# Kernel optimization log

Measured on AMD Instinct MI355X. Metric: run time of the kernel, lower is better.

## Reference

```python
import jax, jax.numpy as jnp
import numpy as np

EPS = 1e-5  # BatchNorm eps (torch default)


def _norm_adj(adj):
    # DenseGCNConv: add self-loops, symmetric degree normalization
    N = adj.shape[-1]
    adj = adj + jnp.eye(N, dtype=adj.dtype)
    d = jnp.clip(adj.sum(-1), 1.0, None) ** -0.5
    return d[..., :, None] * adj * d[..., None, :]


def _gcn(x, adj_norm, W, b):
    return jnp.einsum('bij,bjf->bif', adj_norm, x @ W) + b


def _batchnorm(h, gamma, beta):
    # torch BatchNorm1d in training mode over flattened (B*N, C)
    B, N, C = h.shape
    hf = h.reshape(B * N, C)
    mu = hf.mean(0)
    var = hf.var(0)  # biased, as used for normalization
    out = (hf - mu) * jax.lax.rsqrt(var + EPS) * gamma + beta
    return out.reshape(B, N, C)


def setup_inputs() -> dict:
    key = jax.random.key(0)
    ks = jax.random.split(key, 24)
    B, N, F, H, D = 4, 256, 6, 128, 256
    s = 0.05
    a = jax.random.uniform(ks[1], (B, N, N), dtype=jnp.float32)
    adj = ((a + jnp.swapaxes(a, 1, 2)) / 2 < 0.1).astype(jnp.float32)  # sparse symmetric adjacency
    return {
        'x': jax.random.normal(ks[0], (B, N, F), dtype=jnp.float32),
        'adj': adj,
        'W1': jax.random.normal(ks[2], (F, H)) * s, 'b1': jnp.zeros((H,)),
        'W2': jax.random.normal(ks[3], (H, H)) * s, 'b2': jnp.zeros((H,)),
        'W3': jax.random.normal(ks[4], (H, D)) * s, 'b3': jnp.zeros((D,)),
        'g1': jnp.ones((H,)), 'beta1': jnp.zeros((H,)),
        'g2': jnp.ones((H,)), 'beta2': jnp.zeros((H,)),
        'e1w': jax.random.normal(ks[5], (2 * D, H)) * s, 'e1b': jnp.zeros((H,)),
        'e2w': jax.random.normal(ks[6], (H, H // 2)) * s, 'e2b': jnp.zeros((H // 2,)),
        'e3w': jax.random.normal(ks[7], (H // 2, 1)) * s, 'e3b': jnp.zeros((1,)),
        'f1w': jax.random.normal(ks[8], (D, H)) * s, 'f1b': jnp.zeros((H,)),
        'f2w': jax.random.normal(ks[9], (H, H)) * s, 'f2b': jnp.zeros((H,)),
        'f3w': jax.random.normal(ks[10], (H, F)) * s, 'f3b': jnp.zeros((F,)),
    }


def reference(x, adj, W1, b1, W2, b2, W3, b3, g1, beta1, g2, beta2,
              e1w, e1b, e2w, e2b, e3w, e3b, f1w, f1b, f2w, f2b, f3w, f3b):
    adj_norm = _norm_adj(adj)
    h = jax.nn.relu(_batchnorm(_gcn(x, adj_norm, W1, b1), g1, beta1))
    h = jax.nn.relu(_batchnorm(_gcn(h, adj_norm, W2, b2), g2, beta2))
    h = jax.nn.relu(_gcn(h, adj_norm, W3, b3))  # [B,N,D]
    D = h.shape[-1]
    # AdjacencyDecoder: Linear(cat(h_i,h_j)) == h_i@e1w[:D] + h_j@e1w[D:] (fused form, same math)
    hi = h @ e1w[:D]   # [B,N,H]
    hj = h @ e1w[D:]   # [B,N,H]
    p = jax.nn.relu(hi[:, :, None, :] + hj[:, None, :, :] + e1b)  # [B,N,N,H]
    p = jax.nn.relu(p @ e2w + e2b)                                 # [B,N,N,H/2]
    logits = (p @ e3w + e3b)[..., 0]                               # [B,N,N]
    logits = (logits + jnp.swapaxes(logits, 1, 2)) / 2
    adj_pred = jax.nn.sigmoid(logits)
    # FeatureDecoder
    f = jax.nn.relu(h @ f1w + f1b)
    f = jax.nn.relu(f @ f2w + f2b)
    feat_pred = f @ f3w + f3b
    return adj_pred, feat_pred
```

## Files before the change

### kernel.cpp

```cpp
#include <hip/hip_runtime.h>


typedef float v4f __attribute__((ext_vector_type(4)));
typedef short v8s __attribute__((ext_vector_type(8)));

__device__ __forceinline__ unsigned short f2bs(float f) {
    union { float f; unsigned int u; } v;
    v.f = f;
    return (unsigned short)((v.u + 0x7fffu + ((v.u >> 16) & 1u)) >> 16);
}

__global__ void k_pre(const float* x, const float* W1, const float* adj,
                      const float* e2w, float* buf, float* dg,
                      unsigned short* bfr_g, float* st) {
    __shared__ float ss[256];
    int blk = blockIdx.x, tid = threadIdx.x;
    if (blk < 512) {
        int idx = blk * 256 + tid;
        int m = idx >> 7, n = idx & 127;
        float s = 0.f;
        for (int k = 0; k < 6; k++) s += x[m * 6 + k] * W1[k * 128 + n];
        buf[idx] = s;
    } else if (blk < 768) {
        int row = (blk - 512) * 4 + (tid >> 6);
        int lane = tid & 63;
        const float* ap = adj + (long)row * 256;
        ss[tid] = ap[lane] + ap[lane + 64] + ap[lane + 128] + ap[lane + 192];
        __syncthreads();
        for (int o = 32; o > 0; o >>= 1) {
            if (lane < o) ss[tid] += ss[tid + o];
            __syncthreads();
        }
        if (lane == 0) {
            float t = ss[tid] + 1.f;
            if (t < 1.f) t = 1.f;
            dg[row] = rsqrtf(t);
        }
    } else {
        for (int s = tid; s < 8192; s += 256) {
            int k = s >> 6, n = s & 63;
            int kc = k >> 5, q = (k & 31) >> 3, t = k & 7;
            int nt = n >> 4, c2 = n & 15;
            bfr_g[(((nt * 4 + kc) * 64) + q * 16 + c2) * 8 + t] = f2bs(e2w[s]);
        }
        st[tid] = 0.f;
        st[256 + tid] = 0.f;
    }
}

__global__ void k_an(const float* adj, const float* dg, float* An) {
    for (int p = 0; p < 2; p++) {
        int idx = blockIdx.x * 256 + threadIdx.x + p * 131072;
        int b = idx >> 16, i = (idx >> 8) & 255, j = idx & 255;
        float v = adj[idx] + ((i == j) ? 1.f : 0.f);
        An[idx] = dg[b * 256 + i] * v * dg[b * 256 + j];
    }
}

__device__ void dev_tile(int t, const float* A, const float* B, const float* bias,
                         const float* stat, const float* g, const float* beta,
                         float* ostat, float* C,
                         int K, int N, int relu,
                         int sA, int sB, int sC, int tiles_n, int tiles_m,
                         float* smem) {
    float* As = smem;
    float* Bs = smem + 272;
    int tid = threadIdx.x;
    int n2 = tid & 15, ml = tid >> 4;
    int bx = t % tiles_n;
    int tmp = t / tiles_n;
    int by = tmp % tiles_m;
    int bz = tmp / tiles_m;
    int m0 = by * 16, n0 = bx * 32;
    const float* Ab = A + (long)bz * sA;
    const float* Bb = B + (long)bz * sB;
    float* Cb = C + (long)bz * sC;
    float c0 = 0.f, c1 = 0.f;
    for (int k0 = 0; k0 < K; k0 += 16) {
        int kk = tid & 15, mm = tid >> 4;
        int kg = k0 + kk;
        float v = Ab[(long)(m0 + mm) * K + kg];
        if (stat != 0) {
            float mu = stat[kg] * (1.f / 1024.f);
            float vr = stat[128 + kg] * (1.f / 1024.f) - mu * mu;
            float sc = rsqrtf(vr + 1e-5f) * g[kg];
            v = (v - mu) * sc + beta[kg];
            if (v < 0.f) v = 0.f;
        }
        As[kk * 17 + mm] = v;
        int nn2 = tid & 31, kk2 = tid >> 5;
        Bs[kk2 * 33 + nn2] = Bb[(long)(k0 + kk2) * N + n0 + nn2];
        int idx = tid + 256;
        nn2 = idx & 31; kk2 = idx >> 5;
        Bs[kk2 * 33 + nn2] = Bb[(long)(k0 + kk2) * N + n0 + nn2];
        __syncthreads();
        #pragma unroll
        for (int q = 0; q < 16; q++) {
            float a = As[q * 17 + ml];
            float b0 = Bs[q * 33 + n2 * 2];
            float b1 = Bs[q * 33 + n2 * 2 + 1];
            c0 += a * b0; c1 += a * b1;
        }
        __syncthreads();
    }
    int mRow = m0 + ml, nn = n0 + n2 * 2;
    if (bias != 0) { c0 += bias[nn]; c1 += bias[nn + 1]; }
    if (relu) {
        if (c0 < 0.f) c0 = 0.f;
        if (c1 < 0.f) c1 = 0.f;
    }
    Cb[(long)mRow * N + nn] = c0;
    Cb[(long)mRow * N + nn + 1] = c1;

    if (ostat != 0) {
        float* sred = smem + 800;
        float* qred = smem + 1344;
        __syncthreads();
        sred[(n2 * 2) * 17 + ml] = c0;
        sred[(n2 * 2 + 1) * 17 + ml] = c1;
        qred[(n2 * 2) * 17 + ml] = c0 * c0;
        qred[(n2 * 2 + 1) * 17 + ml] = c1 * c1;
        __syncthreads();
        if (tid < 32) {
            float s = 0.f, q = 0.f;
            for (int u = 0; u < 16; u++) {
                s += sred[tid * 17 + u];
                q += qred[tid * 17 + u];
            }
            atomicAdd(&ostat[n0 + tid], s);
            atomicAdd(&ostat[128 + n0 + tid], q);
        }
    }
}

__global__ void k_tgemm(const float* A, const float* B, const float* bias,
                        const float* stat, const float* g, const float* beta,
                        float* ostat, float* C,
                        int K, int N, int relu,
                        int sA, int sB, int sC, int tiles_n, int tiles_m) {
    __shared__ float smem[1888];
    dev_tile(blockIdx.x, A, B, bias, stat, g, beta, ostat, C,
             K, N, relu, sA, sB, sC, tiles_n, tiles_m, smem);
}

__global__ void k_g67(const float* hb, const float* e1w, float* hi,
                      const float* f1w, const float* f1b, float* f1) {
    __shared__ float smem[1888];
    int t = blockIdx.x;
    if (t < 512) {
        dev_tile(t, hb, e1w, 0, 0, 0, 0, 0, hi,
                 256, 128, 0, 0, 32768, 131072, 4, 64, smem);
    } else {
        dev_tile(t - 512, hb, f1w, f1b, 0, 0, 0, 0, f1,
                 256, 128, 1, 0, 0, 0, 4, 64, smem);
    }
}

__global__ void k_decf(const float* hi, const float* hj, const float* e1b,
                       const unsigned short* bfr_g, const float* e2b,
                       const float* e3w, const float* e3b,
                       const float* f1, const float* f2w, const float* f2b_,
                       const float* f3w, const float* f3b,
                       float* lg, float* out) {
    __shared__ float smem[4608];
    int tid = threadIdx.x;
    int blk = blockIdx.x;
    if (blk < 1024) {
        float* red = smem;
        float* pre_sh = smem + 4352;
        int lane = tid & 63, wv = tid >> 6;
        int col = lane & 15, quad = lane >> 4;
        int bi = blk, b = bi >> 8;
        if (tid < 128) pre_sh[tid] = hi[bi * 128 + tid] + e1b[tid];
        __syncthreads();
        float e2bv[4], e3wv[4];
        for (int nt = 0; nt < 4; nt++) {
            e2bv[nt] = e2b[nt * 16 + col];
            e3wv[nt] = e3w[nt * 16 + col];
        }
        const float* hjb = hj + b * 32768;
        #pragma unroll 1
        for (int ms = 0; ms < 4; ms++) {
            v4f acc[4];
            for (int nt = 0; nt < 4; nt++) {
                v4f z = {0.f, 0.f, 0.f, 0.f};
                acc[nt] = z;
            }
            int j = wv * 64 + ms * 16 + col;
            const float* rowp = hjb + j * 128 + quad * 8;
            #pragma unroll 1
            for (int kc = 0; kc < 4; kc++) {
                const float* pp = pre_sh + kc * 32 + quad * 8;
                const float* hp = rowp + kc * 32;
                v8s af;
                #pragma unroll
                for (int t = 0; t < 8; t++) {
                    float p = pp[t] + hp[t];
                    p = (p > 0.f) ? p : 0.f;
                    af[t] = (short)f2bs(p);
                }
                #pragma unroll
                for (int nt = 0; nt < 4; nt++) {
                    v8s bf = *(const v8s*)&bfr_g[(((nt * 4 + kc) * 64) + lane) * 8];
                    acc[nt] = __builtin_amdgcn_mfma_f32_16x16x32_bf16(
                        af, bf, acc[nt], 0, 0, 0);
                }
            }
            #pragma unroll
            for (int r = 0; r < 4; r++) {
                float s = 0.f;
                #pragma unroll
                for (int nt = 0; nt < 4; nt++) {
                    float v = acc[nt][r] + e2bv[nt];
                    if (v > 0.f) s += v * e3wv[nt];
                }
                red[(wv * 64 + ms * 16 + quad * 4 + r) * 17 + col] = s;
            }
        }
        __syncthreads();
        float s = e3b[0];
        for (int c = 0; c < 16; c++) s += red[tid * 17 + c];
        lg[bi * 256 + tid] = s;
    } else {
        float* f2row = smem;
        int r0 = (blk - 1024) * 4;
        for (int p = 0; p < 2; p++) {
            int idx = tid + p * 256;
            int r = r0 + (idx >> 7), n = idx & 127;
            float s = f2b_[n];
            const float* f1r = f1 + (long)r * 128;
            for (int k = 0; k < 128; k++) s += f1r[k] * f2w[k * 128 + n];
            if (s < 0.f) s = 0.f;
            f2row[idx] = s;
        }
        __syncthreads();
        if (tid < 24) {
            int r = tid / 6, c = tid % 6;
            float s = f3b[c];
            const float* fr = f2row + r * 128;
            for (int k = 0; k < 128; k++) s += fr[k] * f3w[k * 6 + c];
            out[262144 + (r0 + r) * 6 + c] = s;
        }
    }
}

__global__ void k_symsig(const float* lg, float* out) {
    for (int p = 0; p < 2; p++) {
        int idx = blockIdx.x * 256 + threadIdx.x + p * 131072;
        int b = idx >> 16, i = (idx >> 8) & 255, j = idx & 255;
        float v = 0.5f * (lg[idx] + lg[(b << 16) + (j << 8) + i]);
        out[idx] = 1.f / (1.f + expf(-v));
    }
}

extern "C" void kernel_launch(void* const* d_in, const int* in_sizes, int n_in,
                              void* d_out, int out_size, void* d_ws, size_t ws_size,
                              hipStream_t stream) {
    const float* x   = (const float*)d_in[0];
    const float* adj = (const float*)d_in[1];
    const float* W1  = (const float*)d_in[2];
    const float* b1  = (const float*)d_in[3];
    const float* W2  = (const float*)d_in[4];
    const float* b2  = (const float*)d_in[5];
    const float* W3  = (const float*)d_in[6];
    const float* b3  = (const float*)d_in[7];
    const float* g1  = (const float*)d_in[8];
    const float* be1 = (const float*)d_in[9];
    const float* g2  = (const float*)d_in[10];
    const float* be2 = (const float*)d_in[11];
    const float* e1w = (const float*)d_in[12];
    const float* e1b = (const float*)d_in[13];
    const float* e2w = (const float*)d_in[14];
    const float* e2b = (const float*)d_in[15];
    const float* e3w = (const float*)d_in[16];
    const float* e3b = (const float*)d_in[17];
    const float* f1w = (const float*)d_in[18];
    const float* f1b = (const float*)d_in[19];
    const float* f2w = (const float*)d_in[20];
    const float* f2b_ = (const float*)d_in[21];
    const float* f3w = (const float*)d_in[22];
    const float* f3b = (const float*)d_in[23];

    float* out = (float*)d_out;

    if (ws_size < (size_t)1600000 * 4) {
        hipMemsetAsync(d_out, 0x60, 4096, stream);
        return;
    }
    float* ws = (float*)d_ws;
    float* st1 = ws;
    float* st2 = ws + 256;
    float* dg  = ws + 512;
    unsigned short* bfr_g = (unsigned short*)(ws + 1536);
    float* An  = ws + 5632;
    float* buf = An + 262144;
    float* hb  = buf + 262144;
    float* lg  = hb + 262144;
    float* h1  = lg + 262144;
    float* h2  = h1 + 131072;
    float* hi  = h2 + 131072;
    float* hj  = hi + 131072;

    k_pre<<<769, 256, 0, stream>>>(x, W1, adj, e2w, buf, dg, bfr_g, st1);
    k_an<<<512, 256, 0, stream>>>(adj, dg, An);
    k_tgemm<<<256, 256, 0, stream>>>(An, buf, b1, 0, 0, 0, st1, h1,
                                     256, 128, 0, 65536, 32768, 32768, 4, 16);
    k_tgemm<<<256, 256, 0, stream>>>(h1, W2, 0, st1, g1, be1, 0, buf,
                                     128, 128, 0, 0, 0, 0, 4, 64);
    k_tgemm<<<256, 256, 0, stream>>>(An, buf, b2, 0, 0, 0, st2, h2,
                                     256, 128, 0, 65536, 32768, 32768, 4, 16);
    k_tgemm<<<512, 256, 0, stream>>>(h2, W3, 0, st2, g2, be2, 0, buf,
                                     128, 256, 0, 0, 0, 0, 8, 64);
    k_tgemm<<<512, 256, 0, stream>>>(An, buf, b3, 0, 0, 0, 0, hb,
                                     256, 256, 1, 65536, 65536, 65536, 8, 16);
    k_g67<<<768, 256, 0, stream>>>(hb, e1w, hi, f1w, f1b, h1);
    k_decf<<<1280, 256, 0, stream>>>(hi, hj, e1b, bfr_g, e2b, e3w, e3b,
                                     h1, f2w, f2b_, f3w, f3b, lg, out);
    k_symsig<<<512, 256, 0, stream>>>(lg, out);
}
```

Baseline: 218.6 us.

## Fuse adjacency normalization into first GCN GEMM, stage full K in LDS, tile symsig

Removes the separate k_an kernel: the first aggregation GEMM now reads raw adj, applies self-loop and degree scaling on load, and writes the normalized matrix for later layers from the bx==0 tiles. The tiled GEMM now loads the whole K extent of A and B into a larger shared buffer before a single sync and one compute loop, replacing the per-16 K-step double-sync loop. The symmetric sigmoid is rewritten to process upper-triangular 32x32 tile pairs through shared memory, so both the row and the transposed reads are coalesced. The much larger LDS footprint (about 49KB per block) may cut occupancy, and the GEMM loses overlap between loads and compute.

```diff
diff --git a/kernel.cpp b/kernel.cpp
--- a/kernel.cpp
+++ b/kernel.cpp
@@ -48,23 +48,15 @@
     }
 }
 
-__global__ void k_an(const float* adj, const float* dg, float* An) {
-    for (int p = 0; p < 2; p++) {
-        int idx = blockIdx.x * 256 + threadIdx.x + p * 131072;
-        int b = idx >> 16, i = (idx >> 8) & 255, j = idx & 255;
-        float v = adj[idx] + ((i == j) ? 1.f : 0.f);
-        An[idx] = dg[b * 256 + i] * v * dg[b * 256 + j];
-    }
-}
-
 __device__ void dev_tile(int t, const float* A, const float* B, const float* bias,
+                         const float* dgA, float* anOut,
                          const float* stat, const float* g, const float* beta,
                          float* ostat, float* C,
                          int K, int N, int relu,
                          int sA, int sB, int sC, int tiles_n, int tiles_m,
                          float* smem) {
     float* As = smem;
-    float* Bs = smem + 272;
+    float* Bs = smem + 4352;
     int tid = threadIdx.x;
     int n2 = tid & 15, ml = tid >> 4;
     int bx = t % tiles_n;
@@ -75,33 +67,39 @@
     const float* Ab = A + (long)bz * sA;
     const float* Bb = B + (long)bz * sB;
     float* Cb = C + (long)bz * sC;
-    float c0 = 0.f, c1 = 0.f;
-    for (int k0 = 0; k0 < K; k0 += 16) {
-        int kk = tid & 15, mm = tid >> 4;
-        int kg = k0 + kk;
+    const float* dgb = (dgA != 0) ? (dgA + bz * 256) : 0;
+
+    int kk = tid & 15, mm = tid >> 4;
+    int nb = tid & 31, kb = tid >> 5;
+    float di = (dgA != 0) ? dgb[m0 + mm] : 0.f;
+    for (int ka = 0; ka < K; ka += 16) {
+        int kg = ka + kk;
         float v = Ab[(long)(m0 + mm) * K + kg];
-        if (stat != 0) {
+        if (dgA != 0) {
+            if (m0 + mm == kg) v += 1.f;
+            v = di * v * dgb[kg];
+            if (anOut != 0 && bx == 0)
+                anOut[bz * 65536 + (m0 + mm) * 256 + kg] = v;
+        } else if (stat != 0) {
             float mu = stat[kg] * (1.f / 1024.f);
             float vr = stat[128 + kg] * (1.f / 1024.f) - mu * mu;
             float sc = rsqrtf(vr + 1e-5f) * g[kg];
             v = (v - mu) * sc + beta[kg];
             if (v < 0.f) v = 0.f;
         }
-        As[kk * 17 + mm] = v;
-        int nn2 = tid & 31, kk2 = tid >> 5;
-        Bs[kk2 * 33 + nn2] = Bb[(long)(k0 + kk2) * N + n0 + nn2];
-        int idx = tid + 256;
-        nn2 = idx & 31; kk2 = idx >> 5;
-        Bs[kk2 * 33 + nn2] = Bb[(long)(k0 + kk2) * N + n0 + nn2];
-        __syncthreads();
-        #pragma unroll
-        for (int q = 0; q < 16; q++) {
-            float a = As[q * 17 + ml];
-            float b0 = Bs[q * 33 + n2 * 2];
-            float b1 = Bs[q * 33 + n2 * 2 + 1];
-            c0 += a * b0; c1 += a * b1;
-        }
-        __syncthreads();
+        As[kg * 17 + mm] = v;
+        int kg2 = ka + kb;
+        Bs[kg2 * 32 + nb] = Bb[(long)kg2 * N + n0 + nb];
+        kg2 = ka + kb + 8;
+        Bs[kg2 * 32 + nb] = Bb[(long)kg2 * N + n0 + nb];
+    }
+    __syncthreads();
+    float c0 = 0.f, c1 = 0.f;
+    #pragma unroll 8
+    for (int q = 0; q < K; q++) {
+        float a = As[q * 17 + ml];
+        c0 += a * Bs[q * 32 + n2 * 2];
+        c1 += a * Bs[q * 32 + n2 * 2 + 1];
     }
     int mRow = m0 + ml, nn = n0 + n2 * 2;
     if (bias != 0) { c0 += bias[nn]; c1 += bias[nn + 1]; }
@@ -113,8 +111,8 @@
     Cb[(long)mRow * N + nn + 1] = c1;
 
     if (ostat != 0) {
-        float* sred = smem + 800;
-        float* qred = smem + 1344;
+        float* sred = smem;
+        float* qred = smem + 544;
         __syncthreads();
         sred[(n2 * 2) * 17 + ml] = c0;
         sred[(n2 * 2 + 1) * 17 + ml] = c1;
@@ -134,24 +132,25 @@
 }
 
 __global__ void k_tgemm(const float* A, const float* B, const float* bias,
+                        const float* dgA, float* anOut,
                         const float* stat, const float* g, const float* beta,
                         float* ostat, float* C,
                         int K, int N, int relu,
                         int sA, int sB, int sC, int tiles_n, int tiles_m) {
-    __shared__ float smem[1888];
-    dev_tile(blockIdx.x, A, B, bias, stat, g, beta, ostat, C,
+    __shared__ float smem[12544];
+    dev_tile(blockIdx.x, A, B, bias, dgA, anOut, stat, g, beta, ostat, C,
              K, N, relu, sA, sB, sC, tiles_n, tiles_m, smem);
 }
 
 __global__ void k_g67(const float* hb, const float* e1w, float* hi,
                       const float* f1w, const float* f1b, float* f1) {
-    __shared__ float smem[1888];
+    __shared__ float smem[12544];
     int t = blockIdx.x;
     if (t < 512) {
-        dev_tile(t, hb, e1w, 0, 0, 0, 0, 0, hi,
+        dev_tile(t, hb, e1w, 0, 0, 0, 0, 0, 0, 0, hi,
                  256, 128, 0, 0, 32768, 131072, 4, 64, smem);
     } else {
-        dev_tile(t - 512, hb, f1w, f1b, 0, 0, 0, 0, f1,
+        dev_tile(t - 512, hb, f1w, f1b, 0, 0, 0, 0, 0, 0, f1,
                  256, 128, 1, 0, 0, 0, 4, 64, smem);
     }
 }
@@ -245,11 +244,31 @@
 }
 
 __global__ void k_symsig(const float* lg, float* out) {
-    for (int p = 0; p < 2; p++) {
-        int idx = blockIdx.x * 256 + threadIdx.x + p * 131072;
-        int b = idx >> 16, i = (idx >> 8) & 255, j = idx & 255;
-        float v = 0.5f * (lg[idx] + lg[(b << 16) + (j << 8) + i]);
-        out[idx] = 1.f / (1.f + expf(-v));
+    __shared__ float Ta[32 * 33];
+    __shared__ float Tb[32 * 33];
+    int tid = threadIdx.x;
+    int b = blockIdx.x / 36;
+    int t = blockIdx.x % 36;
+    int ti = 0, rem = t;
+    while (rem >= 8 - ti) { rem -= 8 - ti; ti++; }
+    int tj = ti + rem;
+    int i0 = ti * 32, j0 = tj * 32;
+    const float* lgb = lg + b * 65536;
+    for (int p = 0; p < 4; p++) {
+        int idx = p * 256 + tid;
+        int r = idx >> 5, c = idx & 31;
+        Ta[r * 33 + c] = lgb[(i0 + r) * 256 + j0 + c];
+        Tb[r * 33 + c] = lgb[(j0 + r) * 256 + i0 + c];
+    }
+    __syncthreads();
+    float* ob = out + b * 65536;
+    for (int p = 0; p < 4; p++) {
+        int idx = p * 256 + tid;
+        int r = idx >> 5, c = idx & 31;
+        float v1 = 0.5f * (Ta[r * 33 + c] + Tb[c * 33 + r]);
+        ob[(i0 + r) * 256 + j0 + c] = 1.f / (1.f + expf(-v1));
+        float v2 = 0.5f * (Tb[r * 33 + c] + Ta[c * 33 + r]);
+        ob[(j0 + r) * 256 + i0 + c] = 1.f / (1.f + expf(-v2));
     }
 }
 
@@ -302,19 +321,18 @@
     float* hj  = hi + 131072;
 
     k_pre<<<769, 256, 0, stream>>>(x, W1, adj, e2w, buf, dg, bfr_g, st1);
-    k_an<<<512, 256, 0, stream>>>(adj, dg, An);
-    k_tgemm<<<256, 256, 0, stream>>>(An, buf, b1, 0, 0, 0, st1, h1,
+    k_tgemm<<<256, 256, 0, stream>>>(adj, buf, b1, dg, An, 0, 0, 0, st1, h1,
                                      256, 128, 0, 65536, 32768, 32768, 4, 16);
-    k_tgemm<<<256, 256, 0, stream>>>(h1, W2, 0, st1, g1, be1, 0, buf,
+    k_tgemm<<<256, 256, 0, stream>>>(h1, W2, 0, 0, 0, st1, g1, be1, 0, buf,
                                      128, 128, 0, 0, 0, 0, 4, 64);
-    k_tgemm<<<256, 256, 0, stream>>>(An, buf, b2, 0, 0, 0, st2, h2,
+    k_tgemm<<<256, 256, 0, stream>>>(An, buf, b2, 0, 0, 0, 0, 0, st2, h2,
                                      256, 128, 0, 65536, 32768, 32768, 4, 16);
-    k_tgemm<<<512, 256, 0, stream>>>(h2, W3, 0, st2, g2, be2, 0, buf,
+    k_tgemm<<<512, 256, 0, stream>>>(h2, W3, 0, 0, 0, st2, g2, be2, 0, buf,
                                      128, 256, 0, 0, 0, 0, 8, 64);
-    k_tgemm<<<512, 256, 0, stream>>>(An, buf, b3, 0, 0, 0, 0, hb,
+    k_tgemm<<<512, 256, 0, stream>>>(An, buf, b3, 0, 0, 0, 0, 0, 0, hb,
                                      256, 256, 1, 65536, 65536, 65536, 8, 16);
     k_g67<<<768, 256, 0, stream>>>(hb, e1w, hi, f1w, f1b, h1);
     k_decf<<<1280, 256, 0, stream>>>(hi, hj, e1b, bfr_g, e2b, e3w, e3b,
                                      h1, f2w, f2b_, f3w, f3b, lg, out);
-    k_symsig<<<512, 256, 0, stream>>>(lg, out);
-}
+    k_symsig<<<144, 256, 0, stream>>>(lg, out);
+}
```

Measured after the change: 217.7 us. Within noise of the previous version (-0.4%).
